# Kernel tuning notes

Measured on AMD Instinct MI355X. Metric: run time of the kernel, lower is better.

The kernel has to match this reference:

```python
import jax, jax.numpy as jnp
import numpy as np

B, S, D, T, H = 4, 2048, 1024, 5, 8


def setup_inputs() -> dict:
    key = jax.random.key(0)
    ks = jax.random.split(key, 12)
    sc = 0.02  # small init scale for weights so attention logits stay sane
    return {
        "x": jax.random.normal(ks[0], (B, S, D), jnp.float32),
        "time_steps": jax.random.randint(ks[1], (B, S), 0, T),
        "gamma": jnp.ones((T, D), jnp.float32),
        "beta": jax.random.normal(ks[2], (T, D), jnp.float32) * sc,
        "decay": jnp.ones((T,), jnp.float32),
        "shift_W": jax.random.normal(ks[3], (D, D), jnp.float32) * sc,
        "shift_b": jax.random.normal(ks[4], (D,), jnp.float32) * sc,
        "in_proj_W": jax.random.normal(ks[5], (3 * D, D), jnp.float32) * sc,
        "in_proj_b": jax.random.normal(ks[6], (3 * D,), jnp.float32) * sc,
        "out_proj_W": jax.random.normal(ks[7], (D, D), jnp.float32) * sc,
        "out_proj_b": jax.random.normal(ks[8], (D,), jnp.float32) * sc,
    }


def reference(x, time_steps, gamma, beta, decay, shift_W, shift_b,
              in_proj_W, in_proj_b, out_proj_W, out_proj_b):
    eps = 1e-5
    T_ = gamma.shape[0]
    b_, s_, d_ = x.shape
    hd = d_ // H

    # --- per-token indexed LayerNorm + decay (vectorized gather of norm params) ---
    idx = jnp.clip(time_steps, 0, T_ - 1)              # safe gather index [B,S]
    mu = jnp.mean(x, axis=-1, keepdims=True)
    var = jnp.mean(jnp.square(x - mu), axis=-1, keepdims=True)
    xn = (x - mu) * jax.lax.rsqrt(var + eps)           # [B,S,D]
    normed = (xn * gamma[idx] + beta[idx]) * decay[idx][..., None]
    x = jnp.where((time_steps < T_)[..., None], normed, x)

    # --- residual temporal shift (Linear) ---
    x = x + x @ shift_W.T + shift_b

    # --- torch-style MultiheadAttention(x, x, x), batch_first ---
    qkv = x @ in_proj_W.T + in_proj_b                  # [B,S,3D]
    q, k, v = jnp.split(qkv, 3, axis=-1)
    q = q.reshape(b_, s_, H, hd)
    k = k.reshape(b_, s_, H, hd)
    v = v.reshape(b_, s_, H, hd)
    scale = 1.0 / jnp.sqrt(jnp.asarray(hd, x.dtype))
    scores = jnp.einsum('bqhd,bkhd->bhqk', q, k) * scale   # [B,H,S,S]
    attn = jax.nn.softmax(scores, axis=-1)
    ctx = jnp.einsum('bhqk,bkhd->bqhd', attn, v).reshape(b_, s_, d_)
    attended = ctx @ out_proj_W.T + out_proj_b
    return x + attended
```

## Files before the change

### kernel.cpp

```cpp
#include <hip/hip_runtime.h>
#include <math.h>

#define B_ 4
#define S_ 2048
#define D_ 1024
#define T_ 5
#define H_ 8
#define HD_ 128
#define M_ (B_*S_)

typedef __bf16 bf16x8 __attribute__((ext_vector_type(8)));
typedef float  f32x4  __attribute__((ext_vector_type(4)));

__device__ __forceinline__ float bf2f(unsigned short u) {
    union { unsigned int i; float f; } c; c.i = ((unsigned int)u) << 16; return c.f;
}
__device__ __forceinline__ unsigned short f2bf(float f) {
    union { float f; unsigned int i; } c; c.f = f;
    unsigned int u = c.i;
    u += 0x7fffu + ((u >> 16) & 1u);
    return (unsigned short)(u >> 16);
}

__device__ __forceinline__ void gll16(const void* g, void* l) {
    __builtin_amdgcn_global_load_lds(
        (const __attribute__((address_space(1))) void*)g,
        (__attribute__((address_space(3))) void*)l, 16, 0, 0);
}

__global__ __launch_bounds__(256) void f2bf_kernel(
    const float* __restrict__ src, unsigned short* __restrict__ dst)
{
    int i = (blockIdx.x * 256 + threadIdx.x) * 4;
    float4 v = *(const float4*)(src + i);
    ushort4 o;
    o.x = f2bf(v.x); o.y = f2bf(v.y); o.z = f2bf(v.z); o.w = f2bf(v.w);
    *(ushort4*)(dst + i) = o;
}

__global__ __launch_bounds__(256) void ln_kernel(
    const float* __restrict__ x, const int* __restrict__ ts,
    const float* __restrict__ gamma, const float* __restrict__ beta,
    const float* __restrict__ decay, unsigned short* __restrict__ out)
{
    int row = blockIdx.x;
    int tid = threadIdx.x;
    float4 v = ((const float4*)(x + (size_t)row * D_))[tid];
    float s  = v.x + v.y + v.z + v.w;
    float s2 = v.x*v.x + v.y*v.y + v.z*v.z + v.w*v.w;
    #pragma unroll
    for (int off = 32; off; off >>= 1) {
        s  += __shfl_down(s,  off);
        s2 += __shfl_down(s2, off);
    }
    __shared__ float ps[4], ps2[4];
    if ((tid & 63) == 0) { ps[tid >> 6] = s; ps2[tid >> 6] = s2; }
    __syncthreads();
    float tot  = ps[0]  + ps[1]  + ps[2]  + ps[3];
    float tot2 = ps2[0] + ps2[1] + ps2[2] + ps2[3];
    float mu   = tot  * (1.0f / D_);
    float var  = tot2 * (1.0f / D_) - mu * mu;
    float rstd = rsqrtf(var + 1e-5f);

    int t  = ts[row];
    int tc = min(max(t, 0), T_ - 1);
    float4 g = ((const float4*)(gamma + (size_t)tc * D_))[tid];
    float4 b = ((const float4*)(beta  + (size_t)tc * D_))[tid];
    float dec = decay[tc];

    float4 o;
    o.x = ((v.x - mu) * rstd * g.x + b.x) * dec;
    o.y = ((v.y - mu) * rstd * g.y + b.y) * dec;
    o.z = ((v.z - mu) * rstd * g.z + b.z) * dec;
    o.w = ((v.w - mu) * rstd * g.w + b.w) * dec;
    if (t >= T_) o = v;
    ushort4 ob;
    ob.x = f2bf(o.x); ob.y = f2bf(o.y); ob.z = f2bf(o.z); ob.w = f2bf(o.w);
    ((ushort4*)(out + (size_t)row * D_))[tid] = ob;
}

__global__ __launch_bounds__(256) void gemm_mfma(
    const unsigned short* __restrict__ A,
    const unsigned short* __restrict__ Wt,
    const float* __restrict__ bias,
    const float* __restrict__ ResF,
    const unsigned short* __restrict__ ResB,
    float* __restrict__ Cf,
    unsigned short* __restrict__ Cb,
    int M, int N, int K)
{
    __shared__ __align__(16) unsigned short As[128 * 32];
    __shared__ __align__(16) unsigned short Bs[128 * 32];
    int tid  = threadIdx.x;
    int w    = tid >> 6, lane = tid & 63;
    int lm   = lane & 15, quad = lane >> 4;
    int wm   = w & 1,  wn   = w >> 1;
    int i0 = blockIdx.y * 128, j0 = blockIdx.x * 128;

    f32x4 acc[4][4];
    #pragma unroll
    for (int mt = 0; mt < 4; ++mt)
        #pragma unroll
        for (int nt = 0; nt < 4; ++nt)
            acc[mt][nt] = (f32x4){0.f, 0.f, 0.f, 0.f};

    int c0 = w * 128 + lane;
    int r0 = c0 >> 2,   k80 = (c0 & 3) * 8;
    int c1 = c0 + 64;
    int r1 = c1 >> 2,   k81 = (c1 & 3) * 8;

    for (int kt = 0; kt < K; kt += 32) {
        __syncthreads();
        gll16(A  + (size_t)(i0 + r0) * K + kt + k80, As + (size_t)(w * 128 + 0 ) * 8);
        gll16(A  + (size_t)(i0 + r1) * K + kt + k81, As + (size_t)(w * 128 + 64) * 8);
        gll16(Wt + (size_t)(j0 + r0) * K + kt + k80, Bs + (size_t)(w * 128 + 0 ) * 8);
        gll16(Wt + (size_t)(j0 + r1) * K + kt + k81, Bs + (size_t)(w * 128 + 64) * 8);
        __syncthreads();

        bf16x8 af[4], bfr[4];
        #pragma unroll
        for (int mt = 0; mt < 4; ++mt)
            af[mt] = *(const bf16x8*)&As[(wm * 64 + mt * 16 + lm) * 32 + quad * 8];
        #pragma unroll
        for (int nt = 0; nt < 4; ++nt)
            bfr[nt] = *(const bf16x8*)&Bs[(wn * 64 + nt * 16 + lm) * 32 + quad * 8];
        #pragma unroll
        for (int mt = 0; mt < 4; ++mt)
            #pragma unroll
            for (int nt = 0; nt < 4; ++nt)
                acc[mt][nt] = __builtin_amdgcn_mfma_f32_16x16x32_bf16(
                    af[mt], bfr[nt], acc[mt][nt], 0, 0, 0);
    }

    #pragma unroll
    for (int nt = 0; nt < 4; ++nt) {
        int j = j0 + wn * 64 + nt * 16 + lm;
        float bj = bias[j];
        #pragma unroll
        for (int mt = 0; mt < 4; ++mt) {
            #pragma unroll
            for (int r = 0; r < 4; ++r) {
                int i = i0 + wm * 64 + mt * 16 + quad * 4 + r;
                size_t off = (size_t)i * N + j;
                float v = acc[mt][nt][r] + bj;
                if (ResF) v += ResF[off];
                else if (ResB) v += bf2f(ResB[off]);
                if (Cf) Cf[off] = v;
                if (Cb) Cb[off] = f2bf(v);
            }
        }
    }
}

__global__ __launch_bounds__(256) void transpose_v(
    const unsigned short* __restrict__ qkv, unsigned short* __restrict__ vt)
{
    __shared__ unsigned short Ts[64][72];
    int t = threadIdx.x;
    int s0 = blockIdx.x * 64, c0 = blockIdx.y * 64, b = blockIdx.z;
    int r  = t >> 2, cg = (t & 3) * 16;
    const unsigned short* src =
        qkv + (size_t)(b * S_ + s0 + r) * (3 * D_) + 2 * D_ + c0 + cg;
    *(bf16x8*)&Ts[r][cg]     = *(const bf16x8*)(src);
    *(bf16x8*)&Ts[r][cg + 8] = *(const bf16x8*)(src + 8);
    __syncthreads();
    int dd = t >> 2, sg = (t & 3) * 16;
    unsigned short tmp[16];
    #pragma unroll
    for (int j = 0; j < 16; ++j) tmp[j] = Ts[sg + j][dd];
    unsigned short* dst = vt + ((size_t)b * D_ + c0 + dd) * S_ + s0 + sg;
    *(bf16x8*)dst       = *(bf16x8*)&tmp[0];
    *(bf16x8*)(dst + 8) = *(bf16x8*)&tmp[8];
}

__global__ __launch_bounds__(256, 2) void flash_mfma(
    const unsigned short* __restrict__ qkv,
    const unsigned short* __restrict__ vt,
    unsigned short* __restrict__ ctx)
{
    __shared__ unsigned short Ks [64][136];
    __shared__ unsigned short Vts[128][72];
    __shared__ unsigned short Ps [4][32][72];

    int tid  = threadIdx.x;
    int w    = tid >> 6, lane = tid & 63;
    int lm   = lane & 15, quad = lane >> 4;
    int qt = blockIdx.x, h = blockIdx.y, b = blockIdx.z;
    const int rs = 3 * D_;
    const float scale = 0.08838834764831844f;
    size_t qbase  = (size_t)b * S_ * rs + (size_t)h * HD_;
    size_t kbase  = qbase + D_;
    size_t vtbase = ((size_t)b * H_ + h) * (size_t)HD_ * S_;
    int q0 = qt * 128 + w * 32;

    bf16x8 qf[2][4];
    #pragma unroll
    for (int mt = 0; mt < 2; ++mt)
        #pragma unroll
        for (int kc = 0; kc < 4; ++kc) {
            bf16x8 raw = *(const bf16x8*)(
                qkv + qbase + (size_t)(q0 + mt * 16 + lm) * rs + kc * 32 + quad * 8);
            bf16x8 sc;
            #pragma unroll
            for (int j = 0; j < 8; ++j) {
                unsigned short u;
                __builtin_memcpy(&u, (const char*)&raw + 2 * j, 2);
                u = f2bf(bf2f(u) * scale);
                __builtin_memcpy((char*)&sc + 2 * j, &u, 2);
            }
            qf[mt][kc] = sc;
        }

    f32x4 oacc[2][8];
    #pragma unroll
    for (int mt = 0; mt < 2; ++mt)
        #pragma unroll
        for (int n = 0; n < 8; ++n)
            oacc[mt][n] = (f32x4){0.f, 0.f, 0.f, 0.f};
    float lst[2][4];
    #pragma unroll
    for (int mt = 0; mt < 2; ++mt)
        #pragma unroll
        for (int r = 0; r < 4; ++r) lst[mt][r] = 0.f;

    for (int kt = 0; kt < S_ / 64; ++kt) {
        int k0 = kt * 64;
        __syncthreads();
        #pragma unroll
        for (int i = 0; i < 4; ++i) {
            int chunk = tid + 256 * i;
            int r = chunk >> 4, cc = chunk & 15;
            bf16x8 kv8 = *(const bf16x8*)(
                qkv + kbase + (size_t)(k0 + r) * rs + cc * 8);
            *(bf16x8*)&Ks[r][cc * 8] = kv8;
        }
        #pragma unroll
        for (int i = 0; i < 4; ++i) {
            int chunk = tid + 256 * i;
            int d = chunk >> 3, cc = chunk & 7;
            bf16x8 vv8 = *(const bf16x8*)(
                vt + vtbase + (size_t)d * S_ + k0 + cc * 8);
            *(bf16x8*)&Vts[d][cc * 8] = vv8;
        }
        __syncthreads();

        f32x4 sacc[2][4];
        #pragma unroll
        for (int mt = 0; mt < 2; ++mt)
            #pragma unroll
            for (int n = 0; n < 4; ++n)
                sacc[mt][n] = (f32x4){0.f, 0.f, 0.f, 0.f};
        #pragma unroll
        for (int n = 0; n < 4; ++n) {
            bf16x8 bk[4];
            #pragma unroll
            for (int kc = 0; kc < 4; ++kc)
                bk[kc] = *(const bf16x8*)&Ks[n * 16 + lm][kc * 32 + quad * 8];
            #pragma unroll
            for (int mt = 0; mt < 2; ++mt)
                #pragma unroll
                for (int kc = 0; kc < 4; ++kc)
                    sacc[mt][n] = __builtin_amdgcn_mfma_f32_16x16x32_bf16(
                        qf[mt][kc], bk[kc], sacc[mt][n], 0, 0, 0);
        }

        #pragma unroll
        for (int mt = 0; mt < 2; ++mt) {
            #pragma unroll
            for (int r = 0; r < 4; ++r) {
                float p0 = __expf(sacc[mt][0][r]);
                float p1 = __expf(sacc[mt][1][r]);
                float p2 = __expf(sacc[mt][2][r]);
                float p3 = __expf(sacc[mt][3][r]);
                lst[mt][r] += (p0 + p1) + (p2 + p3);
                int row = mt * 16 + quad * 4 + r;
                Ps[w][row][ 0 + lm] = f2bf(p0);
                Ps[w][row][16 + lm] = f2bf(p1);
                Ps[w][row][32 + lm] = f2bf(p2);
                Ps[w][row][48 + lm] = f2bf(p3);
            }
        }

        bf16x8 pa[2][2];
        #pragma unroll
        for (int mt = 0; mt < 2; ++mt)
            #pragma unroll
            for (int kc = 0; kc < 2; ++kc)
                pa[mt][kc] = *(const bf16x8*)&Ps[w][mt * 16 + lm][kc * 32 + quad * 8];
        #pragma unroll
        for (int n = 0; n < 8; ++n) {
            bf16x8 bv0 = *(const bf16x8*)&Vts[n * 16 + lm][quad * 8];
            bf16x8 bv1 = *(const bf16x8*)&Vts[n * 16 + lm][32 + quad * 8];
            #pragma unroll
            for (int mt = 0; mt < 2; ++mt) {
                oacc[mt][n] = __builtin_amdgcn_mfma_f32_16x16x32_bf16(
                    pa[mt][0], bv0, oacc[mt][n], 0, 0, 0);
                oacc[mt][n] = __builtin_amdgcn_mfma_f32_16x16x32_bf16(
                    pa[mt][1], bv1, oacc[mt][n], 0, 0, 0);
            }
        }
    }

    float linv[2][4];
    #pragma unroll
    for (int mt = 0; mt < 2; ++mt)
        #pragma unroll
        for (int r = 0; r < 4; ++r) {
            float l = lst[mt][r];
            l += __shfl_xor(l, 1);
            l += __shfl_xor(l, 2);
            l += __shfl_xor(l, 4);
            l += __shfl_xor(l, 8);
            linv[mt][r] = 1.0f / l;
        }
    size_t rowbase = (size_t)b * S_ + (size_t)qt * 128 + w * 32;
    #pragma unroll
    for (int mt = 0; mt < 2; ++mt)
        #pragma unroll
        for (int r = 0; r < 4; ++r) {
            size_t row = rowbase + mt * 16 + quad * 4 + r;
            unsigned short* dst = ctx + row * D_ + h * HD_ + lm;
            #pragma unroll
            for (int n = 0; n < 8; ++n)
                dst[n * 16] = f2bf(oacc[mt][n][r] * linv[mt][r]);
        }
}

extern "C" void kernel_launch(void* const* d_in, const int* in_sizes, int n_in,
                              void* d_out, int out_size, void* d_ws, size_t ws_size,
                              hipStream_t stream) {
    (void)in_sizes; (void)n_in; (void)out_size; (void)ws_size;
    const float* x          = (const float*)d_in[0];
    const int*   ts         = (const int*)  d_in[1];
    const float* gamma      = (const float*)d_in[2];
    const float* beta       = (const float*)d_in[3];
    const float* decay      = (const float*)d_in[4];
    const float* shift_W    = (const float*)d_in[5];
    const float* shift_b    = (const float*)d_in[6];
    const float* in_proj_W  = (const float*)d_in[7];
    const float* in_proj_b  = (const float*)d_in[8];
    const float* out_proj_W = (const float*)d_in[9];
    const float* out_proj_b = (const float*)d_in[10];
    float* out = (float*)d_out;

    unsigned short* p     = (unsigned short*)d_ws;
    unsigned short* xln_b = p;
    unsigned short* qkv_b = xln_b + (size_t)M_ * D_;
    unsigned short* xs_b  = qkv_b + (size_t)M_ * 3 * D_;
    unsigned short* wsh_b = xs_b  + (size_t)M_ * D_;
    unsigned short* wip_b = wsh_b + (size_t)D_ * D_;
    unsigned short* wop_b = wip_b + (size_t)3 * D_ * D_;
    unsigned short* vt_b  = xs_b;
    unsigned short* ctx_b = xln_b;
    float* xs = out;

    f2bf_kernel<<<D_ * D_ / 1024,     256, 0, stream>>>(shift_W,    wsh_b);
    f2bf_kernel<<<3 * D_ * D_ / 1024, 256, 0, stream>>>(in_proj_W,  wip_b);
    f2bf_kernel<<<D_ * D_ / 1024,     256, 0, stream>>>(out_proj_W, wop_b);

    ln_kernel<<<M_, 256, 0, stream>>>(x, ts, gamma, beta, decay, xln_b);

    gemm_mfma<<<dim3(D_ / 128, M_ / 128), 256, 0, stream>>>(
        xln_b, wsh_b, shift_b, nullptr, xln_b, xs, xs_b, M_, D_, D_);
    gemm_mfma<<<dim3(3 * D_ / 128, M_ / 128), 256, 0, stream>>>(
        xs_b, wip_b, in_proj_b, nullptr, nullptr, nullptr, qkv_b, M_, 3 * D_, D_);

    transpose_v<<<dim3(S_ / 64, D_ / 64, B_), 256, 0, stream>>>(qkv_b, vt_b);
    flash_mfma<<<dim3(S_ / 128, H_, B_), 256, 0, stream>>>(qkv_b, vt_b, ctx_b);

    gemm_mfma<<<dim3(D_ / 128, M_ / 128), 256, 0, stream>>>(
        ctx_b, wop_b, out_proj_b, xs, nullptr, out, nullptr, M_, D_, D_);
}
```

Baseline: 409.5 us.

## Double-buffer K/V tiles via async global-to-LDS loads with XOR swizzle

```diff
diff --git a/kernel.cpp b/kernel.cpp
--- a/kernel.cpp
+++ b/kernel.cpp
@@ -16,10 +16,8 @@
     union { unsigned int i; float f; } c; c.i = ((unsigned int)u) << 16; return c.f;
 }
 __device__ __forceinline__ unsigned short f2bf(float f) {
-    union { float f; unsigned int i; } c; c.f = f;
-    unsigned int u = c.i;
-    u += 0x7fffu + ((u >> 16) & 1u);
-    return (unsigned short)(u >> 16);
+    __bf16 h = (__bf16)f;
+    unsigned short u; __builtin_memcpy(&u, &h, 2); return u;
 }
 
 __device__ __forceinline__ void gll16(const void* g, void* l) {
@@ -178,21 +176,36 @@
     const unsigned short* __restrict__ vt,
     unsigned short* __restrict__ ctx)
 {
-    __shared__ unsigned short Ks [64][136];
-    __shared__ unsigned short Vts[128][72];
-    __shared__ unsigned short Ps [4][32][72];
+    __shared__ __align__(16) unsigned short Ks [2][64 * 128];
+    __shared__ __align__(16) unsigned short Vts[2][128 * 64];
+    __shared__ __align__(16) unsigned short Ps [4][32 * 64];
 
     int tid  = threadIdx.x;
     int w    = tid >> 6, lane = tid & 63;
     int lm   = lane & 15, quad = lane >> 4;
     int qt = blockIdx.x, h = blockIdx.y, b = blockIdx.z;
     const int rs = 3 * D_;
-    const float scale = 0.08838834764831844f;
+    const float scale = 0.08838834764831844f * 1.4426950408889634f;
     size_t qbase  = (size_t)b * S_ * rs + (size_t)h * HD_;
     size_t kbase  = qbase + D_;
     size_t vtbase = ((size_t)b * H_ + h) * (size_t)HD_ * S_;
     int q0 = qt * 128 + w * 32;
 
+    int krow0 = w * 4 + (lane >> 4);
+    int kcolE = ((((lane & 15) * 16) ^ ((krow0 & 7) << 4)) >> 1);
+    int vrow0 = w * 8 + (lane >> 3);
+    int vcolE = ((((lane & 7)  * 16) ^ ((vrow0 & 7) << 4)) >> 1);
+
+    const int rxor = (lm & 7) << 4;
+
+    #pragma unroll
+    for (int i = 0; i < 4; ++i) {
+        gll16(qkv + kbase + (size_t)(krow0 + 16 * i) * rs + kcolE,
+              &Ks[0][i * 2048 + w * 512]);
+        gll16(vt  + vtbase + (size_t)(vrow0 + 32 * i) * S_ + vcolE,
+              &Vts[0][i * 2048 + w * 512]);
+    }
+
     bf16x8 qf[2][4];
     #pragma unroll
     for (int mt = 0; mt < 2; ++mt)
@@ -202,12 +215,8 @@
                 qkv + qbase + (size_t)(q0 + mt * 16 + lm) * rs + kc * 32 + quad * 8);
             bf16x8 sc;
             #pragma unroll
-            for (int j = 0; j < 8; ++j) {
-                unsigned short u;
-                __builtin_memcpy(&u, (const char*)&raw + 2 * j, 2);
-                u = f2bf(bf2f(u) * scale);
-                __builtin_memcpy((char*)&sc + 2 * j, &u, 2);
-            }
+            for (int j = 0; j < 8; ++j)
+                sc[j] = (__bf16)((float)raw[j] * scale);
             qf[mt][kc] = sc;
         }
 
@@ -223,26 +232,23 @@
         #pragma unroll
         for (int r = 0; r < 4; ++r) lst[mt][r] = 0.f;
 
+    int cur = 0;
     for (int kt = 0; kt < S_ / 64; ++kt) {
-        int k0 = kt * 64;
         __syncthreads();
-        #pragma unroll
-        for (int i = 0; i < 4; ++i) {
-            int chunk = tid + 256 * i;
-            int r = chunk >> 4, cc = chunk & 15;
-            bf16x8 kv8 = *(const bf16x8*)(
-                qkv + kbase + (size_t)(k0 + r) * rs + cc * 8);
-            *(bf16x8*)&Ks[r][cc * 8] = kv8;
-        }
-        #pragma unroll
-        for (int i = 0; i < 4; ++i) {
-            int chunk = tid + 256 * i;
-            int d = chunk >> 3, cc = chunk & 7;
-            bf16x8 vv8 = *(const bf16x8*)(
-                vt + vtbase + (size_t)d * S_ + k0 + cc * 8);
-            *(bf16x8*)&Vts[d][cc * 8] = vv8;
-        }
-        __syncthreads();
+
+        if (kt + 1 < S_ / 64) {
+            int k0n = (kt + 1) * 64, nb = cur ^ 1;
+            #pragma unroll
+            for (int i = 0; i < 4; ++i) {
+                gll16(qkv + kbase + (size_t)(k0n + krow0 + 16 * i) * rs + kcolE,
+                      &Ks[nb][i * 2048 + w * 512]);
+                gll16(vt  + vtbase + (size_t)(vrow0 + 32 * i) * S_ + k0n + vcolE,
+                      &Vts[nb][i * 2048 + w * 512]);
+            }
+        }
+
+        const char* Kb = (const char*)&Ks[cur][0];
+        const char* Vb = (const char*)&Vts[cur][0];
 
         f32x4 sacc[2][4];
         #pragma unroll
@@ -250,12 +256,14 @@
             #pragma unroll
             for (int n = 0; n < 4; ++n)
                 sacc[mt][n] = (f32x4){0.f, 0.f, 0.f, 0.f};
+        __builtin_amdgcn_s_setprio(1);
         #pragma unroll
         for (int n = 0; n < 4; ++n) {
             bf16x8 bk[4];
             #pragma unroll
             for (int kc = 0; kc < 4; ++kc)
-                bk[kc] = *(const bf16x8*)&Ks[n * 16 + lm][kc * 32 + quad * 8];
+                bk[kc] = *(const bf16x8*)(Kb + (n * 16 + lm) * 256 +
+                                          ((kc * 64 + quad * 16) ^ rxor));
             #pragma unroll
             for (int mt = 0; mt < 2; ++mt)
                 #pragma unroll
@@ -263,21 +271,25 @@
                     sacc[mt][n] = __builtin_amdgcn_mfma_f32_16x16x32_bf16(
                         qf[mt][kc], bk[kc], sacc[mt][n], 0, 0, 0);
         }
-
+        __builtin_amdgcn_s_setprio(0);
+
+        char* Pw = (char*)&Ps[w][0];
         #pragma unroll
         for (int mt = 0; mt < 2; ++mt) {
             #pragma unroll
             for (int r = 0; r < 4; ++r) {
-                float p0 = __expf(sacc[mt][0][r]);
-                float p1 = __expf(sacc[mt][1][r]);
-                float p2 = __expf(sacc[mt][2][r]);
-                float p3 = __expf(sacc[mt][3][r]);
+                float p0 = exp2f(sacc[mt][0][r]);
+                float p1 = exp2f(sacc[mt][1][r]);
+                float p2 = exp2f(sacc[mt][2][r]);
+                float p3 = exp2f(sacc[mt][3][r]);
                 lst[mt][r] += (p0 + p1) + (p2 + p3);
                 int row = mt * 16 + quad * 4 + r;
-                Ps[w][row][ 0 + lm] = f2bf(p0);
-                Ps[w][row][16 + lm] = f2bf(p1);
-                Ps[w][row][32 + lm] = f2bf(p2);
-                Ps[w][row][48 + lm] = f2bf(p3);
+                int wx  = (row & 7) << 4;
+                char* rowp = Pw + row * 128;
+                *(unsigned short*)(rowp + (( 0 + lm * 2) ^ wx)) = f2bf(p0);
+                *(unsigned short*)(rowp + ((32 + lm * 2) ^ wx)) = f2bf(p1);
+                *(unsigned short*)(rowp + ((64 + lm * 2) ^ wx)) = f2bf(p2);
+                *(unsigned short*)(rowp + ((96 + lm * 2) ^ wx)) = f2bf(p3);
             }
         }
 
@@ -286,11 +298,15 @@
         for (int mt = 0; mt < 2; ++mt)
             #pragma unroll
             for (int kc = 0; kc < 2; ++kc)
-                pa[mt][kc] = *(const bf16x8*)&Ps[w][mt * 16 + lm][kc * 32 + quad * 8];
+                pa[mt][kc] = *(const bf16x8*)(Pw + (mt * 16 + lm) * 128 +
+                                              ((kc * 64 + quad * 16) ^ rxor));
+        __builtin_amdgcn_s_setprio(1);
         #pragma unroll
         for (int n = 0; n < 8; ++n) {
-            bf16x8 bv0 = *(const bf16x8*)&Vts[n * 16 + lm][quad * 8];
-            bf16x8 bv1 = *(const bf16x8*)&Vts[n * 16 + lm][32 + quad * 8];
+            bf16x8 bv0 = *(const bf16x8*)(Vb + (n * 16 + lm) * 128 +
+                                          (( 0 + quad * 16) ^ rxor));
+            bf16x8 bv1 = *(const bf16x8*)(Vb + (n * 16 + lm) * 128 +
+                                          ((64 + quad * 16) ^ rxor));
             #pragma unroll
             for (int mt = 0; mt < 2; ++mt) {
                 oacc[mt][n] = __builtin_amdgcn_mfma_f32_16x16x32_bf16(
@@ -299,6 +315,8 @@
                     pa[mt][1], bv1, oacc[mt][n], 0, 0, 0);
             }
         }
+        __builtin_amdgcn_s_setprio(0);
+        cur ^= 1;
     }
 
     float linv[2][4];
```

Measured after the change: 412.2 us. No clear change (+0.6%).
